# Kernel tuning notes

Measured on AMD Instinct MI355X. Metric: run time of the kernel, lower is better.

Reference implementation:

```python
import jax, jax.numpy as jnp
import numpy as np

N, IN, HID, OUT = 8192, 512, 256, 128

def setup_inputs() -> dict:
    key = jax.random.key(0)
    k1, k2, k3, k4 = jax.random.split(key, 4)
    adj = jax.random.uniform(k1, (N, N), dtype=jnp.float32)
    feature = jax.random.normal(k2, (N, IN), dtype=jnp.float32)
    W1 = jax.random.normal(k3, (IN, HID), dtype=jnp.float32) * (1.0 / np.sqrt(IN))
    b1 = jnp.zeros((HID,), dtype=jnp.float32)
    W2 = jax.random.normal(k4, (HID, OUT), dtype=jnp.float32) * (1.0 / np.sqrt(HID))
    b2 = jnp.zeros((OUT,), dtype=jnp.float32)
    return {"adj": adj, "feature": feature, "W1": W1, "b1": b1, "W2": W2, "b2": b2}

def reference(adj, feature, W1, b1, W2, b2):
    # GCN encoder: layer1 (relu) then layer2 (linear output)
    h = jax.nn.relu(adj @ (feature @ W1) + b1)   # [N, HID]
    h = adj @ (h @ W2) + b2                      # [N, OUT]
    # InnerProductDecoder: sigmoid(flatten(h @ h.T))
    logits = h @ h.T                             # [N, N]
    h_noise = jax.nn.sigmoid(logits.reshape(-1)) # [N*N]
    return (h_noise, h)
```

## Files before the change

### kernel.cpp

```cpp
#include <hip/hip_runtime.h>


typedef __bf16 bf16x8_t __attribute__((ext_vector_type(8)));
typedef __bf16 bf16x4_t __attribute__((ext_vector_type(4)));
typedef float  f32x4_t  __attribute__((ext_vector_type(4)));

#define MFMA_BF16(a, b, c) __builtin_amdgcn_mfma_f32_16x16x32_bf16((a), (b), (c), 0, 0, 0)

__device__ __forceinline__ bf16x8_t cvt8(f32x4_t u, f32x4_t v) {
    bf16x8_t o;
    o[0] = (__bf16)u[0]; o[1] = (__bf16)u[1]; o[2] = (__bf16)u[2]; o[3] = (__bf16)u[3];
    o[4] = (__bf16)v[0]; o[5] = (__bf16)v[1]; o[6] = (__bf16)v[2]; o[7] = (__bf16)v[3];
    return o;
}

__device__ __forceinline__ f32x4_t nt_load4(const float* p) {
    return __builtin_nontemporal_load((const f32x4_t*)p);
}
__device__ __forceinline__ void nt_store4(f32x4_t v, float* p) {
    __builtin_nontemporal_store(v, (f32x4_t*)p);
}

template<int AUX>
__device__ __forceinline__ void gload_lds16(const float* g, float* l) {
    __builtin_amdgcn_global_load_lds(
        (const __attribute__((address_space(1))) unsigned int*)g,
        (__attribute__((address_space(3))) unsigned int*)l, 16, 0, AUX);
}

__global__ __launch_bounds__(256) void cast_all(
    const float* __restrict__ feat, const float* __restrict__ W1,
    const float* __restrict__ W2, __bf16* __restrict__ fb,
    __bf16* __restrict__ w1t, __bf16* __restrict__ w2t)
{
    const int j = blockIdx.x * 256 + threadIdx.x;
    if (j < 524288) {
        const float* p = feat + (size_t)j * 8;
        f32x4_t u = nt_load4(p);
        f32x4_t v = nt_load4(p + 4);
        *(bf16x8_t*)(fb + (size_t)j * 8) = cvt8(u, v);
    } else if (j < 524288 + 131072) {
        int t = j - 524288;
        int k = t >> 8, n = t & 255;
        w1t[n * 512 + k] = (__bf16)W1[t];
    } else if (j < 524288 + 131072 + 32768) {
        int t = j - 655360;
        int k = t >> 7, n = t & 127;
        w2t[n * 256 + k] = (__bf16)W2[t];
    }
}

template<int MT, int WC>
__global__ __launch_bounds__(256, 2) void gemm_bt_cbf16(
    const __bf16* __restrict__ X, const __bf16* __restrict__ Yb,
    __bf16* __restrict__ C, int K, int N)
{
    constexpr int WR = 4 / WC;
    constexpr int BM = WR * MT * 16;
    constexpr int BN = WC * 64;
    const int mblk = blockIdx.x, nblk = blockIdx.y;
    const int w = threadIdx.x >> 6, lane = threadIdx.x & 63;
    const int wr = w / WC, wc = w % WC;
    const int q = lane >> 4, l16 = lane & 15;
    const int mbase = mblk * BM + wr * (MT * 16);
    const int nbase = nblk * BN + wc * 64;

    f32x4_t acc[MT][4];
    const f32x4_t z = {0.f, 0.f, 0.f, 0.f};
#pragma unroll
    for (int i = 0; i < MT; i++)
#pragma unroll
        for (int jj = 0; jj < 4; jj++) acc[i][jj] = z;

    const __bf16* Xr[MT];
    const __bf16* Yr[4];
#pragma unroll
    for (int i = 0; i < MT; i++) Xr[i] = X + (size_t)(mbase + i * 16 + l16) * K + q * 8;
#pragma unroll
    for (int jj = 0; jj < 4; jj++) Yr[jj] = Yb + (size_t)(nbase + jj * 16 + l16) * K + q * 8;

    for (int k = 0; k < K; k += 32) {
        bf16x8_t a[MT], b[4];
#pragma unroll
        for (int i = 0; i < MT; i++) a[i] = *(const bf16x8_t*)(Xr[i] + k);
#pragma unroll
        for (int jj = 0; jj < 4; jj++) b[jj] = *(const bf16x8_t*)(Yr[jj] + k);
#pragma unroll
        for (int i = 0; i < MT; i++)
#pragma unroll
            for (int jj = 0; jj < 4; jj++) acc[i][jj] = MFMA_BF16(a[i], b[jj], acc[i][jj]);
    }

#pragma unroll
    for (int i = 0; i < MT; i++)
#pragma unroll
        for (int jj = 0; jj < 4; jj++) {
            const int row0 = mbase + i * 16 + q * 4;
            const int col = nbase + jj * 16 + l16;
#pragma unroll
            for (int r = 0; r < 4; r++)
                C[(size_t)(row0 + r) * N + col] = (__bf16)acc[i][jj][r];
        }
}

template<int NN>
__global__ __launch_bounds__(512, 2) void gemm_adj_lds(
    const float* __restrict__ A, const __bf16* __restrict__ Y,
    float* __restrict__ P)
{
    constexpr int NT = NN / 128;
    constexpr int KCH = 4096;
    constexpr int NTILES = KCH / 128;
    __shared__ float As[2][8192];

    const int id = blockIdx.x;
    const int ks = id & 1;
    const int mblk = id >> 1;
    const int w = threadIdx.x >> 6, lane = threadIdx.x & 63;
    const int q = lane >> 4, l16 = lane & 15;
    const int kbase = ks * KCH;

    const int lr = lane >> 5;
    const int lg = lane & 31;
    const float* gsrc[4];
    int loff[4];
#pragma unroll
    for (int j = 0; j < 4; j++) {
        const int row = j * 16 + w * 2 + lr;
        const int colswz = ((lg ^ (row & 31)) << 2);
        gsrc[j] = A + (size_t)(mblk * 64 + row) * 8192 + kbase + colswz;
        loff[j] = row * 128 + (lg << 2);
    }

    const __bf16* Yr[NT];
#pragma unroll
    for (int jj = 0; jj < NT; jj++)
        Yr[jj] = Y + (size_t)(w * (NN / 8) + jj * 16 + l16) * 8192 + q * 8;

    f32x4_t acc[4][NT];
    const f32x4_t z = {0.f, 0.f, 0.f, 0.f};
#pragma unroll
    for (int i = 0; i < 4; i++)
#pragma unroll
        for (int jj = 0; jj < NT; jj++) acc[i][jj] = z;

#pragma unroll
    for (int j = 0; j < 4; j++) gload_lds16<2>(gsrc[j], &As[0][0] + loff[j]);

    int buf = 0;
    for (int kt = 0; kt < NTILES; kt++) {
        const int kk = kbase + (kt << 7);

        bf16x8_t breg[4][NT];
#pragma unroll
        for (int s = 0; s < 4; s++)
#pragma unroll
            for (int jj = 0; jj < NT; jj++)
                breg[s][jj] = *(const bf16x8_t*)(Yr[jj] + kk + s * 32);

        __syncthreads();

        if (kt + 1 < NTILES) {
            const int koff = (kt + 1) << 7;
#pragma unroll
            for (int j = 0; j < 4; j++)
                gload_lds16<2>(gsrc[j] + koff, &As[buf ^ 1][0] + loff[j]);
        }

        const float* __restrict__ L = &As[buf][0];
#pragma unroll
        for (int s = 0; s < 4; s++) {
            bf16x8_t a[4];
#pragma unroll
            for (int i = 0; i < 4; i++) {
                const int r = i * 16 + l16;
                const int g0 = ((s * 8 + q * 2) ^ (r & 31)) << 2;
                const int g1 = ((s * 8 + q * 2 + 1) ^ (r & 31)) << 2;
                f32x4_t u = *(const f32x4_t*)(L + r * 128 + g0);
                f32x4_t v = *(const f32x4_t*)(L + r * 128 + g1);
                a[i] = cvt8(u, v);
            }
#pragma unroll
            for (int i = 0; i < 4; i++)
#pragma unroll
                for (int jj = 0; jj < NT; jj++)
                    acc[i][jj] = MFMA_BF16(a[i], breg[s][jj], acc[i][jj]);
        }
        buf ^= 1;
    }

#pragma unroll
    for (int i = 0; i < 4; i++) {
        const int row0 = mblk * 64 + i * 16 + q * 4;
#pragma unroll
        for (int r = 0; r < 4; r++) {
            float* pp = P + ((size_t)ks * 8192 + row0 + r) * NN + w * (NN / 8) + l16;
#pragma unroll
            for (int jj = 0; jj < NT; jj++)
                __builtin_nontemporal_store(acc[i][jj][r], pp + jj * 16);
        }
    }
}

__global__ __launch_bounds__(256) void epi_relu_bias(
    const float* __restrict__ P, const float* __restrict__ bias,
    __bf16* __restrict__ H)
{
    const size_t SL = (size_t)8192 * 256;
    const size_t idx = ((size_t)blockIdx.x * 256 + threadIdx.x) * 4;
    f32x4_t s0 = nt_load4(P + idx);
    f32x4_t s1 = nt_load4(P + SL + idx);
    const int col = (int)(idx & 255);
    f32x4_t bb = *(const f32x4_t*)(bias + col);
    bf16x4_t o;
#pragma unroll
    for (int e = 0; e < 4; e++)
        o[e] = (__bf16)fmaxf(s0[e] + s1[e] + bb[e], 0.f);
    *(bf16x4_t*)(H + idx) = o;
}

__global__ __launch_bounds__(256) void epi_bias_out(
    const float* __restrict__ P, const float* __restrict__ bias,
    float* __restrict__ Hout, __bf16* __restrict__ Hbf)
{
    const size_t SL = (size_t)8192 * 128;
    const size_t idx = ((size_t)blockIdx.x * 256 + threadIdx.x) * 4;
    f32x4_t s0 = nt_load4(P + idx);
    f32x4_t s1 = nt_load4(P + SL + idx);
    const int col = (int)(idx & 127);
    f32x4_t bb = *(const f32x4_t*)(bias + col);
    f32x4_t o;
#pragma unroll
    for (int e = 0; e < 4; e++)
        o[e] = s0[e] + s1[e] + bb[e];
    nt_store4(o, Hout + idx);
    bf16x4_t ob;
#pragma unroll
    for (int e = 0; e < 4; e++) ob[e] = (__bf16)o[e];
    *(bf16x4_t*)(Hbf + idx) = ob;
}

__global__ __launch_bounds__(256, 4) void gemm_sig(
    const __bf16* __restrict__ H, float* __restrict__ out)
{
    __shared__ float S[64 * 132];

    const int mblk = blockIdx.x, nblk = blockIdx.y;
    const int w = threadIdx.x >> 6, lane = threadIdx.x & 63;
    const int wr = w >> 1, wc = w & 1;
    const int q = lane >> 4, l16 = lane & 15;
    const int mbase = mblk * 128 + wr * 64;
    const int nbase = nblk * 128 + wc * 64;

    f32x4_t acc[4][4];
    const f32x4_t z = {0.f, 0.f, 0.f, 0.f};
#pragma unroll
    for (int i = 0; i < 4; i++)
#pragma unroll
        for (int jj = 0; jj < 4; jj++) acc[i][jj] = z;

#pragma unroll
    for (int k = 0; k < 128; k += 32) {
        bf16x8_t a[4], b[4];
#pragma unroll
        for (int i = 0; i < 4; i++)
            a[i] = *(const bf16x8_t*)(H + (size_t)(mbase + i * 16 + l16) * 128 + k + q * 8);
#pragma unroll
        for (int jj = 0; jj < 4; jj++)
            b[jj] = *(const bf16x8_t*)(H + (size_t)(nbase + jj * 16 + l16) * 128 + k + q * 8);
#pragma unroll
        for (int i = 0; i < 4; i++)
#pragma unroll
            for (int jj = 0; jj < 4; jj++) acc[i][jj] = MFMA_BF16(a[i], b[jj], acc[i][jj]);
    }

#pragma unroll
    for (int h = 0; h < 2; h++) {
        if (h) __syncthreads();
#pragma unroll
        for (int i = 0; i < 2; i++) {
            const int ii = h * 2 + i;
            const int lrow = wr * 32 + i * 16 + q * 4;
#pragma unroll
            for (int jj = 0; jj < 4; jj++) {
                const int col = wc * 64 + jj * 16 + l16;
#pragma unroll
                for (int r = 0; r < 4; r++) {
                    const float x = acc[ii][jj][r];
                    S[(lrow + r) * 132 + col] = 1.0f / (1.0f + __expf(-x));
                }
            }
        }
        __syncthreads();
#pragma unroll
        for (int it = 0; it < 8; it++) {
            const int gid = it * 256 + (int)threadIdx.x;
            const int lr = gid >> 5;
            const int qd = gid & 31;
            f32x4_t v = *(const f32x4_t*)(S + lr * 132 + qd * 4);
            const int grow = mblk * 128 + (lr >> 5) * 64 + (lr & 31) + h * 32;
            const int gcol = nblk * 128 + qd * 4;
            nt_store4(v, out + (size_t)grow * 8192 + gcol);
        }
    }
}

extern "C" void kernel_launch(void* const* d_in, const int* in_sizes, int n_in,
                              void* d_out, int out_size, void* d_ws, size_t ws_size,
                              hipStream_t stream)
{
    const float* adj  = (const float*)d_in[0];
    const float* feat = (const float*)d_in[1];
    const float* W1   = (const float*)d_in[2];
    const float* b1   = (const float*)d_in[3];
    const float* W2   = (const float*)d_in[4];
    const float* b2   = (const float*)d_in[5];
    float* out = (float*)d_out;

    char* p = (char*)d_ws;
    __bf16* featbf = (__bf16*)p; p += (size_t)8192 * 512 * 2;
    __bf16* W1T    = (__bf16*)p; p += (size_t)256 * 512 * 2;
    __bf16* W2T    = (__bf16*)p; p += (size_t)128 * 256 * 2;
    __bf16* t1T    = (__bf16*)p; p += (size_t)256 * 8192 * 2;
    __bf16* h1     = (__bf16*)p; p += (size_t)8192 * 256 * 2;
    __bf16* t2T    = (__bf16*)p; p += (size_t)128 * 8192 * 2;
    __bf16* hbf    = (__bf16*)p; p += (size_t)8192 * 128 * 2;
    float* part    = (float*)p;

    cast_all<<<2688, 256, 0, stream>>>(feat, W1, W2, featbf, W1T, W2T);
    gemm_bt_cbf16<2, 2><<<dim3(4, 64), 256, 0, stream>>>(W1T, featbf, t1T, 512, 8192);
    gemm_adj_lds<256><<<256, 512, 0, stream>>>(adj, t1T, part);
    epi_relu_bias<<<2048, 256, 0, stream>>>(part, b1, h1);
    gemm_bt_cbf16<2, 2><<<dim3(2, 64), 256, 0, stream>>>(W2T, h1, t2T, 256, 8192);
    gemm_adj_lds<128><<<256, 512, 0, stream>>>(adj, t2T, part);
    epi_bias_out<<<1024, 256, 0, stream>>>(part, b2, out + (size_t)8192 * 8192, hbf);
    gemm_sig<<<dim3(64, 64), 256, 0, stream>>>(hbf, out);
}
```

Baseline: 639.5 us.

## Pre-convert adjacency to bf16 in output scratch and stream bf16 tiles in adj GEMMs

The cast kernel now converts the full fp32 adjacency matrix to bf16, storing it in the not-yet-written output buffer. Both adjacency GEMMs then load bf16 tiles into LDS directly, halving LDS footprint and removing per-tile fp32-to-bf16 conversion. This adds an extra full pass over adj (read fp32, write bf16), so total memory traffic rises in exchange for cheaper GEMM inner loops.

```diff
diff --git a/kernel.cpp b/kernel.cpp
--- a/kernel.cpp
+++ b/kernel.cpp
@@ -22,29 +22,36 @@
 }
 
 template<int AUX>
-__device__ __forceinline__ void gload_lds16(const float* g, float* l) {
+__device__ __forceinline__ void gload_lds16b(const __bf16* g, __bf16* l) {
     __builtin_amdgcn_global_load_lds(
         (const __attribute__((address_space(1))) unsigned int*)g,
         (__attribute__((address_space(3))) unsigned int*)l, 16, 0, AUX);
 }
 
 __global__ __launch_bounds__(256) void cast_all(
-    const float* __restrict__ feat, const float* __restrict__ W1,
-    const float* __restrict__ W2, __bf16* __restrict__ fb,
+    const float* __restrict__ adj, const float* __restrict__ feat,
+    const float* __restrict__ W1, const float* __restrict__ W2,
+    __bf16* __restrict__ adjb, __bf16* __restrict__ fb,
     __bf16* __restrict__ w1t, __bf16* __restrict__ w2t)
 {
     const int j = blockIdx.x * 256 + threadIdx.x;
-    if (j < 524288) {
-        const float* p = feat + (size_t)j * 8;
+    if (j < 8388608) {
+        const float* p = adj + (size_t)j * 8;
         f32x4_t u = nt_load4(p);
         f32x4_t v = nt_load4(p + 4);
-        *(bf16x8_t*)(fb + (size_t)j * 8) = cvt8(u, v);
-    } else if (j < 524288 + 131072) {
-        int t = j - 524288;
+        *(bf16x8_t*)(adjb + (size_t)j * 8) = cvt8(u, v);
+    } else if (j < 8912896) {
+        const int t = j - 8388608;
+        const float* p = feat + (size_t)t * 8;
+        f32x4_t u = nt_load4(p);
+        f32x4_t v = nt_load4(p + 4);
+        *(bf16x8_t*)(fb + (size_t)t * 8) = cvt8(u, v);
+    } else if (j < 9043968) {
+        int t = j - 8912896;
         int k = t >> 8, n = t & 255;
         w1t[n * 512 + k] = (__bf16)W1[t];
-    } else if (j < 524288 + 131072 + 32768) {
-        int t = j - 655360;
+    } else if (j < 9076736) {
+        int t = j - 9043968;
         int k = t >> 7, n = t & 127;
         w2t[n * 256 + k] = (__bf16)W2[t];
     }
@@ -105,13 +112,13 @@
 
 template<int NN>
 __global__ __launch_bounds__(512, 2) void gemm_adj_lds(
-    const float* __restrict__ A, const __bf16* __restrict__ Y,
+    const __bf16* __restrict__ Ab, const __bf16* __restrict__ Y,
     float* __restrict__ P)
 {
     constexpr int NT = NN / 128;
     constexpr int KCH = 4096;
     constexpr int NTILES = KCH / 128;
-    __shared__ float As[2][8192];
+    __shared__ __bf16 As[2][8192];
 
     const int id = blockIdx.x;
     const int ks = id & 1;
@@ -120,16 +127,16 @@
     const int q = lane >> 4, l16 = lane & 15;
     const int kbase = ks * KCH;
 
-    const int lr = lane >> 5;
-    const int lg = lane & 31;
-    const float* gsrc[4];
-    int loff[4];
-#pragma unroll
-    for (int j = 0; j < 4; j++) {
-        const int row = j * 16 + w * 2 + lr;
-        const int colswz = ((lg ^ (row & 31)) << 2);
-        gsrc[j] = A + (size_t)(mblk * 64 + row) * 8192 + kbase + colswz;
-        loff[j] = row * 128 + (lg << 2);
+    const int srow = (lane >> 4);
+    const int lg = lane & 15;
+    const __bf16* gsrc[2];
+    int loff[2];
+#pragma unroll
+    for (int j = 0; j < 2; j++) {
+        const int row = j * 32 + w * 4 + srow;
+        const int colswz = (lg ^ (row & 15)) * 8;
+        gsrc[j] = Ab + (size_t)(mblk * 64 + row) * 8192 + kbase + colswz;
+        loff[j] = row * 128 + lg * 8;
     }
 
     const __bf16* Yr[NT];
@@ -145,7 +152,7 @@
         for (int jj = 0; jj < NT; jj++) acc[i][jj] = z;
 
 #pragma unroll
-    for (int j = 0; j < 4; j++) gload_lds16<2>(gsrc[j], &As[0][0] + loff[j]);
+    for (int j = 0; j < 2; j++) gload_lds16b<0>(gsrc[j], &As[0][0] + loff[j]);
 
     int buf = 0;
     for (int kt = 0; kt < NTILES; kt++) {
@@ -163,22 +170,19 @@
         if (kt + 1 < NTILES) {
             const int koff = (kt + 1) << 7;
 #pragma unroll
-            for (int j = 0; j < 4; j++)
-                gload_lds16<2>(gsrc[j] + koff, &As[buf ^ 1][0] + loff[j]);
-        }
-
-        const float* __restrict__ L = &As[buf][0];
+            for (int j = 0; j < 2; j++)
+                gload_lds16b<0>(gsrc[j] + koff, &As[buf ^ 1][0] + loff[j]);
+        }
+
+        const __bf16* __restrict__ L = &As[buf][0];
 #pragma unroll
         for (int s = 0; s < 4; s++) {
             bf16x8_t a[4];
 #pragma unroll
             for (int i = 0; i < 4; i++) {
                 const int r = i * 16 + l16;
-                const int g0 = ((s * 8 + q * 2) ^ (r & 31)) << 2;
-                const int g1 = ((s * 8 + q * 2 + 1) ^ (r & 31)) << 2;
-                f32x4_t u = *(const f32x4_t*)(L + r * 128 + g0);
-                f32x4_t v = *(const f32x4_t*)(L + r * 128 + g1);
-                a[i] = cvt8(u, v);
+                const int g = ((s * 4 + q) ^ (r & 15)) * 8;
+                a[i] = *(const bf16x8_t*)(L + r * 128 + g);
             }
 #pragma unroll
             for (int i = 0; i < 4; i++)
@@ -316,6 +320,8 @@
     const float* W2   = (const float*)d_in[4];
     const float* b2   = (const float*)d_in[5];
     float* out = (float*)d_out;
+
+    __bf16* adjb = (__bf16*)out;
 
     char* p = (char*)d_ws;
     __bf16* featbf = (__bf16*)p; p += (size_t)8192 * 512 * 2;
@@ -327,12 +333,12 @@
     __bf16* hbf    = (__bf16*)p; p += (size_t)8192 * 128 * 2;
     float* part    = (float*)p;
 
-    cast_all<<<2688, 256, 0, stream>>>(feat, W1, W2, featbf, W1T, W2T);
+    cast_all<<<35456, 256, 0, stream>>>(adj, feat, W1, W2, adjb, featbf, W1T, W2T);
     gemm_bt_cbf16<2, 2><<<dim3(4, 64), 256, 0, stream>>>(W1T, featbf, t1T, 512, 8192);
-    gemm_adj_lds<256><<<256, 512, 0, stream>>>(adj, t1T, part);
+    gemm_adj_lds<256><<<256, 512, 0, stream>>>(adjb, t1T, part);
     epi_relu_bias<<<2048, 256, 0, stream>>>(part, b1, h1);
     gemm_bt_cbf16<2, 2><<<dim3(2, 64), 256, 0, stream>>>(W2T, h1, t2T, 256, 8192);
-    gemm_adj_lds<128><<<256, 512, 0, stream>>>(adj, t2T, part);
+    gemm_adj_lds<128><<<256, 512, 0, stream>>>(adjb, t2T, part);
     epi_bias_out<<<1024, 256, 0, stream>>>(part, b2, out + (size_t)8192 * 8192, hbf);
     gemm_sig<<<dim3(64, 64), 256, 0, stream>>>(hbf, out);
 }
```

Result: slower. 665.3 us (+4.0%).
